# Kernel tuning notes

Measured on AMD Instinct MI355X. Metric: run time of the kernel, lower is better.

## Reference

```python
import jax, jax.numpy as jnp
import numpy as np

B, N, D, H = 4, 2048, 768, 12
HD = D // H
SCALE = HD ** -0.5


def setup_inputs() -> dict:
    key = jax.random.key(0)
    k1, k2, k3 = jax.random.split(key, 3)
    x = jax.random.normal(k1, (B, N, D), dtype=jnp.float32)
    w_qkv = jax.random.normal(k2, (D, 3 * D), dtype=jnp.float32) * (D ** -0.5)
    w_proj = jax.random.normal(k3, (D, D), dtype=jnp.float32) * (D ** -0.5)
    b_proj = jnp.zeros((D,), dtype=jnp.float32)
    return {"x": x, "w_qkv": w_qkv, "w_proj": w_proj, "b_proj": b_proj}


def reference(x, w_qkv, w_proj, b_proj):
    b, n, d = x.shape
    qkv = x @ w_qkv                      # [b, n, 3d]
    q, k, v = jnp.split(qkv, 3, axis=-1)
    # [b, n, d] -> [b, h, n, hd]
    split_heads = lambda t: t.reshape(b, n, H, HD).transpose(0, 2, 1, 3)
    q, k, v = split_heads(q), split_heads(k), split_heads(v)
    dots = jnp.einsum('bhqd,bhkd->bhqk', q, k) * SCALE   # [b, h, n, n]
    attn = jax.nn.softmax(dots, axis=-1)
    q_attn = attn[:, :, 0, :]            # attention row of query token 0: [b, h, n]
    # dropout p=0 (eval) -> identity
    out = jnp.einsum('bhqk,bhkd->bhqd', attn, v)          # [b, h, n, hd]
    out = out.transpose(0, 2, 1, 3).reshape(b, n, d)      # [b, n, d]
    return out @ w_proj + b_proj, q_attn
```

## Files before the change

### kernel.cpp

```cpp
#include <hip/hip_runtime.h>


typedef unsigned short u16;
typedef __attribute__((ext_vector_type(8))) short bf8;
typedef __attribute__((ext_vector_type(4))) short bf4;
typedef __attribute__((ext_vector_type(4))) float f4;

#define MFMA16(a, b, c) __builtin_amdgcn_mfma_f32_16x16x32_bf16((a), (b), (c), 0, 0, 0)

#if __has_builtin(__builtin_amdgcn_exp2f)
#define EXP2(x) __builtin_amdgcn_exp2f(x)
#else
#define EXP2(x) __expf((x) * 0.6931471805599453f)
#endif

__device__ __forceinline__ float b2f(u16 h) {
  union { unsigned u; float f; } v; v.u = ((unsigned)h) << 16; return v.f;
}
__device__ __forceinline__ u16 f2b(float f) {
  union { float f; unsigned u; } v; v.f = f;
  unsigned r = v.u + 0x7fffu + ((v.u >> 16) & 1u);
  return (u16)(r >> 16);
}
__device__ __forceinline__ u16 f2bt(float f) {
  union { float f; unsigned u; } v; v.f = f;
  return (u16)(v.u >> 16);
}
__device__ __forceinline__ void gload16(const u16* g, u16* l) {
  __builtin_amdgcn_global_load_lds(
      (const __attribute__((address_space(1))) void*)g,
      (__attribute__((address_space(3))) void*)l, 16, 0, 0);
}

__global__ __launch_bounds__(256) void detect_dtype(
    const u16* __restrict__ x, unsigned* __restrict__ flag) {
  __shared__ int any;
  if (threadIdx.x == 0) any = 0;
  __syncthreads();
  unsigned b = x[2 * threadIdx.x];
  unsigned e = (b >> 7) & 0xFF;
  if (e >= 0x8E) atomicOr(&any, 1);
  __syncthreads();
  if (threadIdx.x == 0) *flag = (unsigned)(any ? 1 : 0);
}

__global__ __launch_bounds__(256) void convert_bf16(
    const void* __restrict__ in, u16* __restrict__ out, int n,
    const unsigned* __restrict__ flag) {
  const int f32 = (int)*flag;
  for (int i = blockIdx.x * 256 + threadIdx.x; i < n; i += gridDim.x * 256)
    out[i] = f32 ? f2b(((const float*)in)[i]) : ((const u16*)in)[i];
}

__global__ __launch_bounds__(256) void transpose_any(
    const void* __restrict__ in, u16* __restrict__ out, int R, int C,
    const unsigned* __restrict__ flag) {
  __shared__ u16 tile[32][33];
  const int f32 = (int)*flag;
  const int bx = blockIdx.x * 32;
  const int by = blockIdx.y * 32;
  const int tx = threadIdx.x & 31, ty = threadIdx.x >> 5;
#pragma unroll
  for (int i = 0; i < 4; i++) {
    size_t idx = (size_t)(by + ty + i * 8) * C + bx + tx;
    tile[ty + i * 8][tx] = f32 ? f2b(((const float*)in)[idx]) : ((const u16*)in)[idx];
  }
  __syncthreads();
#pragma unroll
  for (int i = 0; i < 4; i++)
    out[(size_t)(bx + ty + i * 8) * R + by + tx] = tile[tx][ty + i * 8];
}

__global__ __launch_bounds__(256) void transpose_v(
    const u16* __restrict__ qkv, u16* __restrict__ Vt) {
  __shared__ u16 tile[64][65];
  const int n0 = blockIdx.x * 64, h = blockIdx.y, b = blockIdx.z;
  {
    const int d = threadIdx.x & 63, nq = threadIdx.x >> 6;
#pragma unroll
    for (int i = 0; i < 16; i++) {
      int n = i * 4 + nq;
      tile[n][d] = qkv[(size_t)(b * 2048 + n0 + n) * 2304 + 1536 + h * 64 + d];
    }
  }
  __syncthreads();
  {
    const int n = threadIdx.x & 63, dq = threadIdx.x >> 6;
    const int n2 = (n & ~31) | (((n >> 2) & 3) << 3) | (((n >> 4) & 1) << 2) | (n & 3);
#pragma unroll
    for (int i = 0; i < 16; i++) {
      int d2 = i * 4 + dq;
      Vt[(size_t)((b * 12 + h) * 64 + d2) * 2048 + n0 + n2] = tile[n][d2];
    }
  }
}

template <int BIAS>
__global__ __launch_bounds__(256) void gemm_bt(
    const u16* __restrict__ A, const u16* __restrict__ Bt,
    const void* __restrict__ bias, void* __restrict__ C,
    int M, int Ncols, int K, const unsigned* __restrict__ outflag) {
  __shared__ alignas(16) u16 Al[128 * 32];
  __shared__ alignas(16) u16 Bl[128 * 32];
  const int t = threadIdx.x;
  const int lane = t & 63, wave = t >> 6;
  const int wr = wave >> 1, wc = wave & 1;
  const int quad = lane >> 4, l16 = lane & 15;
  const int bm = blockIdx.y * 128, bn = blockIdx.x * 128;
  const int f32o = outflag ? (int)*outflag : 0;
  const int grow = lane >> 2, gcol = (lane & 3) * 8;
  f4 acc[4][4] = {};
  for (int k0 = 0; k0 < K; k0 += 32) {
    __syncthreads();
#pragma unroll
    for (int c = 0; c < 2; c++) {
      int chunk = wave * 2 + c;
      int row = chunk * 16 + grow;
      gload16(A + (size_t)(bm + row) * K + k0 + gcol, &Al[chunk * 512]);
      gload16(Bt + (size_t)(bn + row) * K + k0 + gcol, &Bl[chunk * 512]);
    }
    __syncthreads();
    bf8 af[4], bfr[4];
#pragma unroll
    for (int mt = 0; mt < 4; mt++)
      af[mt] = *(const bf8*)&Al[(wr * 64 + mt * 16 + l16) * 32 + quad * 8];
#pragma unroll
    for (int nt = 0; nt < 4; nt++)
      bfr[nt] = *(const bf8*)&Bl[(wc * 64 + nt * 16 + l16) * 32 + quad * 8];
#pragma unroll
    for (int mt = 0; mt < 4; mt++)
#pragma unroll
      for (int nt = 0; nt < 4; nt++)
        acc[mt][nt] = MFMA16(af[mt], bfr[nt], acc[mt][nt]);
  }
#pragma unroll
  for (int mt = 0; mt < 4; mt++) {
    int row = bm + wr * 64 + mt * 16 + quad * 4;
#pragma unroll
    for (int nt = 0; nt < 4; nt++) {
      int col = bn + wc * 64 + nt * 16 + l16;
      float bv = 0.f;
      if (BIAS)
        bv = f32o ? ((const float*)bias)[col] : b2f(((const u16*)bias)[col]);
#pragma unroll
      for (int r = 0; r < 4; r++) {
        size_t idx = (size_t)(row + r) * Ncols + col;
        float v = acc[mt][nt][r] + bv;
        if (f32o) ((float*)C)[idx] = v; else ((u16*)C)[idx] = f2b(v);
      }
    }
  }
}

__global__ __launch_bounds__(256, 3) void flash_attn(
    const u16* __restrict__ qkv, const u16* __restrict__ Vt,
    u16* __restrict__ O, float* __restrict__ qe, float* __restrict__ lout) {
  const int STR = 72;
  __shared__ alignas(16) u16 Kl[64 * 72];
  __shared__ alignas(16) u16 Vl[64 * 72];
  const int t = threadIdx.x, lane = t & 63, wave = t >> 6;
  const int quad = lane >> 4, l16 = lane & 15;
  const int id = blockIdx.x;
  const int bh = (id & 7) + 8 * (id >> 7);
  const int qtile = (id >> 3) & 15;
  const int b = bh / 12, h = bh - b * 12;
  const int q0 = qtile * 128 + wave * 32;
  const bool dumpP = (qe != nullptr) && (qtile == 0) && (wave == 0);
  const float SCALE2 = 0.125f * 1.44269504089f;
  const float M0 = 16.f;
  bf8 qf[2][2];
#pragma unroll
  for (int qt = 0; qt < 2; qt++) {
    const u16* Qr = qkv + (size_t)(b * 2048 + q0 + qt * 16 + l16) * 2304 + h * 64;
    bf8 r0 = *(const bf8*)(Qr + quad * 8);
    bf8 r1 = *(const bf8*)(Qr + 32 + quad * 8);
#pragma unroll
    for (int j = 0; j < 8; j++) {
      qf[qt][0][j] = (short)f2b(b2f((u16)r0[j]) * SCALE2);
      qf[qt][1][j] = (short)f2b(b2f((u16)r1[j]) * SCALE2);
    }
  }
  const u16* Kb = qkv + (size_t)(b * 2048) * 2304 + 768 + h * 64;
  const u16* Vb = Vt + (size_t)((b * 12 + h) * 64) * 2048;
  const int srow = t >> 3, sc8 = (t & 7) * 8;
  const int srow2 = srow + 32;
  f4 o[2][4] = {};
  float lpart[2] = {0.f, 0.f};

  bf8 kreg0 = *(const bf8*)(Kb + (size_t)srow * 2304 + sc8);
  bf8 kreg1 = *(const bf8*)(Kb + (size_t)srow2 * 2304 + sc8);
  bf8 vreg0 = *(const bf8*)(Vb + (size_t)srow * 2048 + sc8);
  bf8 vreg1 = *(const bf8*)(Vb + (size_t)srow2 * 2048 + sc8);

  for (int i = 0; i < 32; i++) {
    __syncthreads();
    *(bf8*)&Kl[srow * STR + sc8] = kreg0;
    *(bf8*)&Kl[srow2 * STR + sc8] = kreg1;
    *(bf8*)&Vl[srow * STR + sc8] = vreg0;
    *(bf8*)&Vl[srow2 * STR + sc8] = vreg1;
    __syncthreads();
    if (i < 31) {
      const u16* Kn = Kb + (size_t)(i * 64 + 64) * 2304;
      const u16* Vn = Vb + (i * 64 + 64);
      kreg0 = *(const bf8*)(Kn + (size_t)srow * 2304 + sc8);
      kreg1 = *(const bf8*)(Kn + (size_t)srow2 * 2304 + sc8);
      vreg0 = *(const bf8*)(Vn + (size_t)srow * 2048 + sc8);
      vreg1 = *(const bf8*)(Vn + (size_t)srow2 * 2048 + sc8);
    }
    bf8 pf[2][2];
#pragma unroll
    for (int kt = 0; kt < 4; kt++) {
      bf8 kf0 = *(const bf8*)&Kl[(kt * 16 + l16) * STR + quad * 8];
      bf8 kf1 = *(const bf8*)&Kl[(kt * 16 + l16) * STR + 32 + quad * 8];
#pragma unroll
      for (int qt = 0; qt < 2; qt++) {
        f4 z = {};
        z = MFMA16(kf0, qf[qt][0], z);
        z = MFMA16(kf1, qf[qt][1], z);
        float e0 = EXP2(z[0] - M0);
        float e1 = EXP2(z[1] - M0);
        float e2 = EXP2(z[2] - M0);
        float e3 = EXP2(z[3] - M0);
        lpart[qt] += (e0 + e1) + (e2 + e3);
        if (qt == 0 && dumpP && l16 == 0) {
          f4 ev = {e0, e1, e2, e3};
          *(f4*)&qe[bh * 2048 + i * 64 + kt * 16 + quad * 4] = ev;
        }
        pf[qt][kt >> 1][(kt & 1) * 4 + 0] = (short)f2bt(e0);
        pf[qt][kt >> 1][(kt & 1) * 4 + 1] = (short)f2bt(e1);
        pf[qt][kt >> 1][(kt & 1) * 4 + 2] = (short)f2bt(e2);
        pf[qt][kt >> 1][(kt & 1) * 4 + 3] = (short)f2bt(e3);
      }
    }
#pragma unroll
    for (int pair = 0; pair < 2; pair++) {
#pragma unroll
      for (int nt = 0; nt < 4; nt++) {
        bf8 vf = *(const bf8*)&Vl[(nt * 16 + l16) * STR + pair * 32 + quad * 8];
        o[0][nt] = MFMA16(vf, pf[0][pair], o[0][nt]);
        o[1][nt] = MFMA16(vf, pf[1][pair], o[1][nt]);
      }
    }
  }
#pragma unroll
  for (int qt = 0; qt < 2; qt++) {
    float l = lpart[qt];
    l += __shfl_xor(l, 16, 64);
    l += __shfl_xor(l, 32, 64);
    if (qt == 0 && dumpP && lane == 0) lout[bh] = l;
    float inv = 1.f / l;
    size_t row = (size_t)(b * 2048 + q0 + qt * 16 + l16) * 768 + h * 64;
#pragma unroll
    for (int nt = 0; nt < 4; nt++) {
      bf4 pk = {(short)f2b(o[qt][nt][0] * inv), (short)f2b(o[qt][nt][1] * inv),
                (short)f2b(o[qt][nt][2] * inv), (short)f2b(o[qt][nt][3] * inv)};
      *(bf4*)&O[row + nt * 16 + quad * 4] = pk;
    }
  }
}

__global__ __launch_bounds__(256) void qattn_norm(
    const float* __restrict__ qe, const float* __restrict__ lout,
    void* __restrict__ out, const unsigned* __restrict__ flag) {
  const int bh = blockIdx.x;
  const int f32o = (int)*flag;
  const float inv = 1.f / lout[bh];
  for (int k = threadIdx.x; k < 2048; k += 256) {
    size_t idx = (size_t)6291456 + (size_t)bh * 2048 + k;
    float v = qe[bh * 2048 + k] * inv;
    if (f32o) ((float*)out)[idx] = v; else ((u16*)out)[idx] = f2b(v);
  }
}

__global__ __launch_bounds__(256) void qattn_row0(
    const u16* __restrict__ qkv, void* __restrict__ out,
    const unsigned* __restrict__ flag) {
  const int bh = blockIdx.x, b = bh / 12, h = bh % 12;
  __shared__ float qs[64];
  __shared__ float sv[2048];
  __shared__ float red[8];
  const int t = threadIdx.x;
  const int f32o = (int)*flag;
  if (t < 64) qs[t] = b2f(qkv[(size_t)(b * 2048) * 2304 + h * 64 + t]);
  __syncthreads();
  float lmax = -1e30f;
  for (int k = t; k < 2048; k += 256) {
    const u16* Kr = qkv + (size_t)(b * 2048 + k) * 2304 + 768 + h * 64;
    float acc = 0.f;
#pragma unroll
    for (int j = 0; j < 8; j++) {
      bf8 kv = *(const bf8*)(Kr + j * 8);
#pragma unroll
      for (int d = 0; d < 8; d++) acc += qs[j * 8 + d] * b2f((u16)kv[d]);
    }
    acc *= 0.125f;
    sv[k] = acc;
    lmax = fmaxf(lmax, acc);
  }
#pragma unroll
  for (int off = 32; off >= 1; off >>= 1) lmax = fmaxf(lmax, __shfl_xor(lmax, off, 64));
  if ((t & 63) == 0) red[t >> 6] = lmax;
  __syncthreads();
  const float bmax = fmaxf(fmaxf(red[0], red[1]), fmaxf(red[2], red[3]));
  float lsum = 0.f;
  for (int k = t; k < 2048; k += 256) {
    float e = __expf(sv[k] - bmax);
    sv[k] = e;
    lsum += e;
  }
#pragma unroll
  for (int off = 32; off >= 1; off >>= 1) lsum += __shfl_xor(lsum, off, 64);
  if ((t & 63) == 0) red[4 + (t >> 6)] = lsum;
  __syncthreads();
  const float inv = 1.f / (red[4] + red[5] + red[6] + red[7]);
  for (int k = t; k < 2048; k += 256) {
    size_t idx = (size_t)6291456 + (size_t)bh * 2048 + k;
    float v = sv[k] * inv;
    if (f32o) ((float*)out)[idx] = v; else ((u16*)out)[idx] = f2b(v);
  }
}

extern "C" void kernel_launch(void* const* d_in, const int* in_sizes, int n_in,
                              void* d_out, int out_size, void* d_ws, size_t ws_size,
                              hipStream_t stream) {
  const void* x_raw      = d_in[0];
  const void* w_qkv_raw  = d_in[1];
  const void* w_proj_raw = d_in[2];
  const void* b_proj_raw = d_in[3];
  char* ws = (char*)d_ws;
  unsigned* flag = (unsigned*)ws;
  u16* xbf    = (u16*)(ws + 256);
  u16* wqkvT  = (u16*)(ws + 12583168);
  u16* wprojT = (u16*)(ws + 16122112);
  u16* qkv    = (u16*)(ws + 17301760);
  u16* Vt     = (u16*)(ws + 55050496);
  float* qe   = (float*)(ws + 67633408);
  float* lout = (float*)(ws + 68026624);
  u16* attn   = xbf;
  const bool fused = ws_size >= 68026816ull;

  detect_dtype<<<1, 256, 0, stream>>>((const u16*)x_raw, flag);
  convert_bf16<<<2048, 256, 0, stream>>>(x_raw, xbf, 6291456, flag);
  transpose_any<<<dim3(2304 / 32, 768 / 32), 256, 0, stream>>>(w_qkv_raw, wqkvT, 768, 2304, flag);
  transpose_any<<<dim3(768 / 32, 768 / 32), 256, 0, stream>>>(w_proj_raw, wprojT, 768, 768, flag);
  gemm_bt<0><<<dim3(2304 / 128, 8192 / 128), 256, 0, stream>>>(
      xbf, wqkvT, nullptr, qkv, 8192, 2304, 768, nullptr);
  transpose_v<<<dim3(2048 / 64, 12, 4), 256, 0, stream>>>(qkv, Vt);
  flash_attn<<<dim3(768), 256, 0, stream>>>(qkv, Vt, attn,
                                            fused ? qe : nullptr,
                                            fused ? lout : nullptr);
  if (fused)
    qattn_norm<<<dim3(48), 256, 0, stream>>>(qe, lout, d_out, flag);
  else
    qattn_row0<<<dim3(48), 256, 0, stream>>>(qkv, d_out, flag);
  gemm_bt<1><<<dim3(768 / 128, 8192 / 128), 256, 0, stream>>>(
      attn, wprojT, b_proj_raw, d_out, 8192, 768, 768, flag);
}
```

Baseline: 241.3 us.

## Double-buffer shared-memory tiles in gemm_bt to overlap loads with MFMA

The GEMM used for the QKV and output projections now keeps two LDS buffers for the A and B tiles. Each iteration prefetches the next K-slice into the idle buffer while MFMAs run on the current one, and one barrier per iteration replaces two. The aim is to hide global-load latency behind compute, at the cost of doubling the kernel's LDS footprint, which can reduce occupancy.

New measurement: 239.2 us. About the same (-0.9%).

```diff
diff --git a/kernel.cpp b/kernel.cpp
--- a/kernel.cpp
+++ b/kernel.cpp
@@ -100,8 +100,8 @@
     const u16* __restrict__ A, const u16* __restrict__ Bt,
     const void* __restrict__ bias, void* __restrict__ C,
     int M, int Ncols, int K, const unsigned* __restrict__ outflag) {
-  __shared__ alignas(16) u16 Al[128 * 32];
-  __shared__ alignas(16) u16 Bl[128 * 32];
+  __shared__ alignas(16) u16 Al[2][128 * 32];
+  __shared__ alignas(16) u16 Bl[2][128 * 32];
   const int t = threadIdx.x;
   const int lane = t & 63, wave = t >> 6;
   const int wr = wave >> 1, wc = wave & 1;
@@ -109,24 +109,31 @@
   const int bm = blockIdx.y * 128, bn = blockIdx.x * 128;
   const int f32o = outflag ? (int)*outflag : 0;
   const int grow = lane >> 2, gcol = (lane & 3) * 8;
+  const int chunk0 = wave * 2, chunk1 = wave * 2 + 1;
+  const int arow0 = chunk0 * 16 + grow, arow1 = chunk1 * 16 + grow;
   f4 acc[4][4] = {};
-  for (int k0 = 0; k0 < K; k0 += 32) {
+  gload16(A + (size_t)(bm + arow0) * K + gcol, &Al[0][chunk0 * 512]);
+  gload16(Bt + (size_t)(bn + arow0) * K + gcol, &Bl[0][chunk0 * 512]);
+  gload16(A + (size_t)(bm + arow1) * K + gcol, &Al[0][chunk1 * 512]);
+  gload16(Bt + (size_t)(bn + arow1) * K + gcol, &Bl[0][chunk1 * 512]);
+  const int NIT = K >> 5;
+  for (int i = 0; i < NIT; i++) {
+    const int cur = i & 1, nxt = cur ^ 1;
     __syncthreads();
-#pragma unroll
-    for (int c = 0; c < 2; c++) {
-      int chunk = wave * 2 + c;
-      int row = chunk * 16 + grow;
-      gload16(A + (size_t)(bm + row) * K + k0 + gcol, &Al[chunk * 512]);
-      gload16(Bt + (size_t)(bn + row) * K + k0 + gcol, &Bl[chunk * 512]);
-    }
-    __syncthreads();
+    if (i + 1 < NIT) {
+      int k0 = (i + 1) << 5;
+      gload16(A + (size_t)(bm + arow0) * K + k0 + gcol, &Al[nxt][chunk0 * 512]);
+      gload16(Bt + (size_t)(bn + arow0) * K + k0 + gcol, &Bl[nxt][chunk0 * 512]);
+      gload16(A + (size_t)(bm + arow1) * K + k0 + gcol, &Al[nxt][chunk1 * 512]);
+      gload16(Bt + (size_t)(bn + arow1) * K + k0 + gcol, &Bl[nxt][chunk1 * 512]);
+    }
     bf8 af[4], bfr[4];
 #pragma unroll
     for (int mt = 0; mt < 4; mt++)
-      af[mt] = *(const bf8*)&Al[(wr * 64 + mt * 16 + l16) * 32 + quad * 8];
+      af[mt] = *(const bf8*)&Al[cur][(wr * 64 + mt * 16 + l16) * 32 + quad * 8];
 #pragma unroll
     for (int nt = 0; nt < 4; nt++)
-      bfr[nt] = *(const bf8*)&Bl[(wc * 64 + nt * 16 + l16) * 32 + quad * 8];
+      bfr[nt] = *(const bf8*)&Bl[cur][(wc * 64 + nt * 16 + l16) * 32 + quad * 8];
 #pragma unroll
     for (int mt = 0; mt < 4; mt++)
 #pragma unroll
```
